# Performance work log

Hardware: AMD Instinct MI355X
Metric: run time of the kernel (lower is better)

Reference implementation:

```python
import jax, jax.numpy as jnp
import numpy as np

NPOINT = 2048
RADIUS = 0.2
NSAMPLE = 64
BN_EPS = 1e-5
MLP = [131, 128, 128, 256]  # 128 features + 3 xyz -> 128 -> 128 -> 256


def fps(xyz, npoint):
    """Furthest point sampling. xyz: (B,N,3) -> inds (B,npoint) int32. First index is 0 (CUDA convention)."""
    B, N, _ = xyz.shape
    dist0 = jnp.full((B, N), 1e10, dtype=xyz.dtype)
    idx0 = jnp.zeros((B,), dtype=jnp.int32)

    def step(carry, _):
        dist, last = carry
        last_pt = jnp.take_along_axis(xyz, last[:, None, None].astype(jnp.int32), axis=1)  # (B,1,3)
        d = jnp.sum((xyz - last_pt) ** 2, axis=-1)  # (B,N)
        dist = jnp.minimum(dist, d)
        nxt = jnp.argmax(dist, axis=1).astype(jnp.int32)
        return (dist, nxt), nxt

    (_, _), rest = jax.lax.scan(step, (dist0, idx0), None, length=npoint - 1)
    return jnp.concatenate([idx0[None, :], rest], axis=0).T  # (B,npoint)


def ball_query(all_xyz, new_xyz, radius, nsample):
    """For each query pick the first (lowest-index) nsample points within radius; pad with first hit.
    all_xyz: (B,Np,3), new_xyz: (B,S,3) -> idx (B,S,nsample) int32."""
    Np = all_xyz.shape[1]
    d2 = jnp.sum((new_xyz[:, :, None, :] - all_xyz[:, None, :, :]) ** 2, axis=-1)  # (B,S,Np)
    key = jnp.where(d2 < radius * radius, jnp.arange(Np, dtype=jnp.int32)[None, None, :], Np)
    topk = -jax.lax.top_k(-key, nsample)[0]  # nsample smallest indices, ascending
    valid = topk < Np
    first = topk[..., :1]
    idx = jnp.where(valid, topk, first)
    return jnp.where(idx >= Np, 0, idx).astype(jnp.int32)


def bn_relu(x, gamma, beta):
    # training-mode BatchNorm over (B,S,K) per channel (last axis), biased variance
    mean = jnp.mean(x, axis=(0, 1, 2), keepdims=True)
    var = jnp.mean((x - mean) ** 2, axis=(0, 1, 2), keepdims=True)
    return jax.nn.relu((x - mean) * jax.lax.rsqrt(var + BN_EPS) * gamma + beta)


def setup_inputs() -> dict:
    key = jax.random.key(0)
    ks = jax.random.split(key, 10)
    B, N, M, C = 4, 16384, 256, 128
    fixed_xyz = jax.random.uniform(ks[0], (B, M, 3), dtype=jnp.float32)
    xyz = jax.random.uniform(ks[1], (B, N, 3), dtype=jnp.float32)
    features = jax.random.normal(ks[2], (B, C, M + N), dtype=jnp.float32)
    W1 = jax.random.normal(ks[3], (MLP[1], MLP[0]), dtype=jnp.float32) * 0.05
    W2 = jax.random.normal(ks[4], (MLP[2], MLP[1]), dtype=jnp.float32) * 0.05
    W3 = jax.random.normal(ks[5], (MLP[3], MLP[2]), dtype=jnp.float32) * 0.05
    g1 = jnp.ones((MLP[1],), jnp.float32); b1 = jnp.zeros((MLP[1],), jnp.float32)
    g2 = jnp.ones((MLP[2],), jnp.float32); b2 = jnp.zeros((MLP[2],), jnp.float32)
    g3 = jnp.ones((MLP[3],), jnp.float32); b3 = jnp.zeros((MLP[3],), jnp.float32)
    return {"fixed_xyz": fixed_xyz, "xyz": xyz, "features": features,
            "W1": W1, "g1": g1, "b1": b1, "W2": W2, "g2": g2, "b2": b2,
            "W3": W3, "g3": g3, "b3": b3}


def reference(fixed_xyz, xyz, features, W1, g1, b1, W2, g2, b2, W3, g3, b3):
    B = xyz.shape[0]
    # FPS on the raw cloud, gather sampled centers, prepend fixed seeds
    inds = fps(xyz, NPOINT)  # (B,npoint)
    sampled = jnp.take_along_axis(xyz, inds[:, :, None], axis=1)  # (B,npoint,3)
    new_xyz = jnp.concatenate([fixed_xyz, sampled], axis=1)       # (B,S,3)
    all_xyz = jnp.concatenate([fixed_xyz, xyz], axis=1)           # (B,Np,3)

    idx = ball_query(all_xyz, new_xyz, RADIUS, NSAMPLE)           # (B,S,K)
    b = jnp.arange(B)[:, None, None]
    grouped_xyz = all_xyz[b, idx] - new_xyz[:, :, None, :]        # (B,S,K,3)
    grouped_xyz = grouped_xyz / RADIUS                            # normalize_xyz=True
    feats_t = jnp.transpose(features, (0, 2, 1))                  # (B,Np,C)
    grouped_feats = feats_t[b, idx]                               # (B,S,K,C)
    h = jnp.concatenate([grouped_xyz, grouped_feats], axis=-1)    # (B,S,K,3+C)

    # Shared MLP: 1x1 conv (no bias) + BN + ReLU per layer
    h = bn_relu(jnp.einsum('bskc,oc->bsko', h, W1), g1, b1)
    h = bn_relu(jnp.einsum('bskc,oc->bsko', h, W2), g2, b2)
    h = bn_relu(jnp.einsum('bskc,oc->bsko', h, W3), g3, b3)

    # max pool over the K (nsample) axis -> (B,Cout,S)
    new_features = jnp.transpose(jnp.max(h, axis=2), (0, 2, 1))
    return new_xyz, new_features, inds
```

## Files before the change

kernel.cpp:

```cpp
#include <hip/hip_runtime.h>
#include <hip/hip_bf16.h>
#include <cstdint>
#include <cstddef>

#define NB 4
#define N_PTS 16384
#define M_FIX 256
#define P_ALL 16640
#define S_TOT 2304
#define NPT 2048
#define KNB 64
#define CH1 128
#define CH3 256
#define NRED 589824.0f
#define ZPB (P_ALL / 64)

typedef float v2f __attribute__((ext_vector_type(2)));

#define OUT_XYZ 0
#define OUT_FEAT 27648
#define OUT_INDS 2386944

#define OFF_ALLX   0ull
#define OFF_STATS  798720ull
#define OFF_BN     1060864ull
#define OFF_MAXZ   1064960ull
#define OFF_MINZ   10502144ull
#define OFF_IDX    19939328ull
#define OFF_ZP     22298624ull
#define OFF_NEWX   39337984ull
#define OFF_INDSI  39448576ull
#define OFF_HIST   1064960ull
#define OFF_OFFS   1073152ull
#define OFF_SX     1081344ull
#define OFF_SY     1343488ull
#define OFF_SZ     1605632ull
#define OFF_SIDX   1867776ull
#define OFF_XYZ4   2129920ull

__device__ __forceinline__ float red16s(float v) {
  v += __shfl_xor(v, 1); v += __shfl_xor(v, 2);
  v += __shfl_xor(v, 4); v += __shfl_xor(v, 8);
  return v;
}
__device__ __forceinline__ float red16mx(float v) {
  v = fmaxf(v, __shfl_xor(v, 1)); v = fmaxf(v, __shfl_xor(v, 2));
  v = fmaxf(v, __shfl_xor(v, 4)); v = fmaxf(v, __shfl_xor(v, 8));
  return v;
}
__device__ __forceinline__ float red16mn(float v) {
  v = fminf(v, __shfl_xor(v, 1)); v = fminf(v, __shfl_xor(v, 2));
  v = fminf(v, __shfl_xor(v, 4)); v = fminf(v, __shfl_xor(v, 8));
  return v;
}
__device__ __forceinline__ float xyzp(float dx, float dy, float dz,
                                      float wx, float wy, float wz) {
  return fmaf(dx, wx, fmaf(dy, wy, __fmul_rn(dz, wz)));
}
__device__ __forceinline__ int mort3(int v) {
  return (v & 1) | ((v & 2) << 1) | ((v & 4) << 2);
}
__device__ __forceinline__ int cell_code(float x, float y, float z) {
  int cx = min(7, max(0, (int)(x * 8.0f)));
  int cy = min(7, max(0, (int)(y * 8.0f)));
  int cz = min(7, max(0, (int)(z * 8.0f)));
  return mort3(cx) | (mort3(cy) << 1) | (mort3(cz) << 2);
}

template <int CTRL, int RM>
__device__ __forceinline__ unsigned long long dppmax(unsigned long long k) {
  int lo = (int)(unsigned)(k & 0xFFFFFFFFull);
  int hi = (int)(unsigned)(k >> 32);
  int sl = __builtin_amdgcn_update_dpp(lo, lo, CTRL, RM, 0xF, false);
  int sh = __builtin_amdgcn_update_dpp(hi, hi, CTRL, RM, 0xF, false);
  unsigned long long s = ((unsigned long long)(unsigned)sh << 32) | (unsigned)sl;
  return (s > k) ? s : k;
}
__device__ __forceinline__ unsigned long long wave_max64(unsigned long long k) {
  k = dppmax<0x111, 0xF>(k);
  k = dppmax<0x112, 0xF>(k);
  k = dppmax<0x114, 0xF>(k);
  k = dppmax<0x118, 0xF>(k);
  k = dppmax<0x142, 0xa>(k);
  k = dppmax<0x143, 0xc>(k);
  return k;
}
__device__ __forceinline__ unsigned long long row_max64(unsigned long long k) {
  k = dppmax<0x111, 0xF>(k);
  k = dppmax<0x112, 0xF>(k);
  k = dppmax<0x114, 0xF>(k);
  k = dppmax<0x118, 0xF>(k);
  return k;
}

__global__ void k_build(const float* __restrict__ fixed, const float* __restrict__ xyz,
                        float* __restrict__ allx, float* __restrict__ newx,
                        float* __restrict__ stats, int* __restrict__ inds_i,
                        int* __restrict__ hist, float4* __restrict__ xyz4) {
  int i = blockIdx.x * 256 + threadIdx.x;
  if (i < NB * P_ALL * 3) {
    int b = i / (P_ALL * 3);
    int r = i % (P_ALL * 3);
    int p = r / 3, c = r % 3;
    float v = (p < M_FIX) ? fixed[((size_t)b * M_FIX + p) * 3 + c]
                          : xyz[((size_t)b * N_PTS + (p - M_FIX)) * 3 + c];
    allx[i] = v;
  }
  if (i < NB * N_PTS) {
    const float* pt = xyz + (size_t)i * 3;
    xyz4[i] = make_float4(pt[0], pt[1], pt[2], 0.f);
  }
  if (i < NB * M_FIX * 3) {
    int b = i / (M_FIX * 3);
    int r = i % (M_FIX * 3);
    newx[(size_t)b * S_TOT * 3 + r] = fixed[(size_t)b * M_FIX * 3 + r];
  }
  if (i < 65536) stats[i] = 0.0f;
  if (i < NB * 512) hist[i] = 0;
  if (i < NB) inds_i[(size_t)i * NPT] = 0;
}

__global__ void k_cell(const float* __restrict__ xyz, int* __restrict__ hist) {
  int i = blockIdx.x * 256 + threadIdx.x;
  int b = i >> 14;
  const float* pt = xyz + (size_t)i * 3;
  int code = cell_code(pt[0], pt[1], pt[2]);
  atomicAdd(&hist[(b << 9) + code], 1);
}

__global__ __launch_bounds__(512) void k_scan(const int* __restrict__ hist,
                                              int* __restrict__ offs) {
  __shared__ int tmp[512];
  int b = blockIdx.x, t = threadIdx.x;
  int h = hist[(b << 9) + t];
  tmp[t] = h;
  __syncthreads();
  for (int o = 1; o < 512; o <<= 1) {
    int v = (t >= o) ? tmp[t - o] : 0;
    __syncthreads();
    tmp[t] += v;
    __syncthreads();
  }
  offs[(b << 9) + t] = tmp[t] - h;
}

__global__ void k_scatter(const float* __restrict__ xyz, int* __restrict__ offs,
                          float* __restrict__ sx, float* __restrict__ sy,
                          float* __restrict__ sz, int* __restrict__ sidx) {
  int i = blockIdx.x * 256 + threadIdx.x;
  int b = i >> 14, p = i & 16383;
  const float* pt = xyz + (size_t)i * 3;
  float x = pt[0], y = pt[1], z = pt[2];
  int code = cell_code(x, y, z);
  int pos = atomicAdd(&offs[(b << 9) + code], 1);
  int o = (b << 14) + pos;
  sx[o] = x; sy[o] = y; sz[o] = z; sidx[o] = p;
}

__global__ __launch_bounds__(1024, 4) void k_fps(const float4* __restrict__ xyz4,
                                                 const float* __restrict__ sx,
                                                 const float* __restrict__ sy,
                                                 const float* __restrict__ sz,
                                                 const int* __restrict__ sidx,
                                                 float* __restrict__ newx,
                                                 int* __restrict__ inds_i,
                                                 const float* __restrict__ feats,
                                                 const float* __restrict__ W1,
                                                 __hip_bfloat16* __restrict__ zp) {
  __shared__ __align__(16) float smem[CH1 * 68 + 32 * 132];
  int t = threadIdx.x;

  if (blockIdx.x >= NB) {
    int bz = blockIdx.x - NB;
    int b = bz / ZPB;
    int p0 = (bz % ZPB) * 64;
    float* a_t = smem;
    float* w_t = smem + CH1 * 68;
    for (int r = t; r < CH1 * 64; r += 1024) {
      int c = r >> 6, p = r & 63;
      a_t[c * 68 + p] = feats[((size_t)b * CH1 + c) * P_ALL + p0 + p];
    }
    int tk = t & 63, to = t >> 6;
    v2f acc[4];
#pragma unroll
    for (int p = 0; p < 4; ++p) acc[p] = (v2f){0.f, 0.f};
    const float* Wg = W1 + 3;
    for (int c0 = 0; c0 < CH1; c0 += 32) {
      __syncthreads();
      for (int r = t; r < 32 * 128; r += 1024) {
        int o = r & 127, c = r >> 7;
        w_t[c * 132 + o] = Wg[(size_t)o * 131 + (c0 + c)];
      }
      __syncthreads();
#pragma unroll 4
      for (int c = 0; c < 32; ++c) {
        float a = a_t[(c0 + c) * 68 + tk];
        v2f w2[4];
        *(float4*)&w2[0] = *(const float4*)&w_t[c * 132 + to * 8];
        *(float4*)&w2[2] = *(const float4*)&w_t[c * 132 + to * 8 + 4];
        v2f a2 = {a, a};
#pragma unroll
        for (int p = 0; p < 4; ++p)
          acc[p] = __builtin_elementwise_fma(a2, w2[p], acc[p]);
      }
    }
    union { __hip_bfloat16 h[8]; uint4 u; } tmp;
#pragma unroll
    for (int j = 0; j < 8; ++j)
      tmp.h[j] = __float2bfloat16((j & 1) ? acc[j >> 1].y : acc[j >> 1].x);
    *(uint4*)&zp[((size_t)b * P_ALL + p0 + tk) * CH1 + to * 8] = tmp.u;
    return;
  }

  unsigned long long* red = (unsigned long long*)smem;
  float4* wcoord = (float4*)(smem + 32);
  float4* s_win = (float4*)(smem + 96);
  int* idxbuf = (int*)(smem + 100);

  int b = blockIdx.x;
  const float4* bx4 = xyz4 + (size_t)b * N_PTS;
  int off0 = (b << 14) + (t << 4);
  v2f px2[8], py2[8], pz2[8];
  float dist[16];
  unsigned npidp[8];
#pragma unroll
  for (int u = 0; u < 8; ++u) {
    px2[u] = *(const v2f*)&sx[off0 + 2 * u];
    py2[u] = *(const v2f*)&sy[off0 + 2 * u];
    pz2[u] = *(const v2f*)&sz[off0 + 2 * u];
    dist[2 * u] = 1e10f; dist[2 * u + 1] = 1e10f;
  }
#pragma unroll
  for (int u = 0; u < 8; ++u) {
    unsigned a = 16383u - (unsigned)sidx[off0 + 2 * u];
    unsigned c = 16383u - (unsigned)sidx[off0 + 2 * u + 1];
    npidp[u] = a | (c << 16);
  }
  float xmn = px2[0].x, xmx = px2[0].x, ymn = py2[0].x, ymx = py2[0].x;
  float zmn = pz2[0].x, zmx = pz2[0].x;
#pragma unroll
  for (int u = 0; u < 8; ++u) {
    xmn = fminf(xmn, fminf(px2[u].x, px2[u].y));
    xmx = fmaxf(xmx, fmaxf(px2[u].x, px2[u].y));
    ymn = fminf(ymn, fminf(py2[u].x, py2[u].y));
    ymx = fmaxf(ymx, fmaxf(py2[u].x, py2[u].y));
    zmn = fminf(zmn, fminf(pz2[u].x, pz2[u].y));
    zmx = fmaxf(zmx, fmaxf(pz2[u].x, pz2[u].y));
  }
  float cx = (xmn + xmx) * 0.5f, cy = (ymn + ymx) * 0.5f, cz = (zmn + zmx) * 0.5f;
  float r2m = 0.f;
#pragma unroll
  for (int u = 0; u < 8; ++u) {
#pragma unroll
    for (int h = 0; h < 2; ++h) {
      float ax = (h ? px2[u].y : px2[u].x) - cx;
      float ay = (h ? py2[u].y : py2[u].x) - cy;
      float az = (h ? pz2[u].y : pz2[u].x) - cz;
      r2m = fmaxf(r2m, ax * ax + ay * ay + az * az);
    }
  }
  float rad = sqrtf(r2m) + 2e-3f;
  float4 p0 = bx4[0];
  float lx = p0.x, ly = p0.y, lz = p0.z;
  if (t == 0) {
    size_t nb0 = ((size_t)b * S_TOT + M_FIX) * 3;
    newx[nb0] = lx; newx[nb0 + 1] = ly; newx[nb0 + 2] = lz;
  }
  unsigned long long bestkey = 0ull;
  unsigned long long kprev = ~0ull;
  float thr = 3.4e38f;
  int lane = t & 63, wid = t >> 6;
  for (int iter = 1; iter < NPT; ++iter) {
    float ex = lx - cx, ey = ly - cy, ez = lz - cz;
    bool active = (ex * ex + ey * ey + ez * ez) < thr;
    if (__ballot(active) != 0ull) {
      bool ch = false;
      if (active) {
#pragma clang fp contract(off)
        v2f l2x = {lx, lx}, l2y = {ly, ly}, l2z = {lz, lz};
#pragma unroll
        for (int u = 0; u < 8; ++u) {
          v2f dx = px2[u] - l2x;
          v2f dy = py2[u] - l2y;
          v2f dz = pz2[u] - l2z;
          v2f xx = dx * dx;
          v2f yy = dy * dy;
          v2f zz = dz * dz;
          v2f d2 = (xx + yy) + zz;
          if (d2.x < dist[2 * u])     { dist[2 * u] = d2.x;     ch = true; }
          if (d2.y < dist[2 * u + 1]) { dist[2 * u + 1] = d2.y; ch = true; }
        }
      }
      if (__ballot(ch) != 0ull) {
        if (ch) {
          unsigned long long c0 = 0ull, c1 = 0ull, c2 = 0ull, c3 = 0ull;
#pragma unroll
          for (int j = 0; j < 16; ++j) {
            unsigned lo16 = (j & 1) ? (npidp[j >> 1] >> 16) : (npidp[j >> 1] & 0xFFFFu);
            unsigned long long kj =
                ((unsigned long long)__float_as_uint(dist[j]) << 32) | lo16;
            if ((j & 3) == 0) c0 = (kj > c0) ? kj : c0;
            else if ((j & 3) == 1) c1 = (kj > c1) ? kj : c1;
            else if ((j & 3) == 2) c2 = (kj > c2) ? kj : c2;
            else c3 = (kj > c3) ? kj : c3;
          }
          c0 = (c1 > c0) ? c1 : c0;
          c2 = (c3 > c2) ? c3 : c2;
          bestkey = (c2 > c0) ? c2 : c0;
          float ub = __uint_as_float((unsigned)(bestkey >> 32));
          float tq = sqrtf(ub) + rad;
          thr = tq * tq;
        }
        unsigned long long k = wave_max64(bestkey);
        unsigned long long kall = __shfl(k, 63);
        if (kall != kprev) {
          if (bestkey == kall) {
            unsigned lo = (unsigned)(kall & 0xFFFFull);
            float wx = 0.f, wy = 0.f, wz = 0.f;
#pragma unroll
            for (int u = 0; u < 8; ++u) {
              unsigned pk = npidp[u];
              if ((pk & 0xFFFFu) == lo) { wx = px2[u].x; wy = py2[u].x; wz = pz2[u].x; }
              if ((pk >> 16) == lo)     { wx = px2[u].y; wy = py2[u].y; wz = pz2[u].y; }
            }
            wcoord[wid] = make_float4(wx, wy, wz, 0.f);
          }
          kprev = kall;
        }
        if (lane == 63) red[wid] = k;
      }
    }
    __syncthreads();
    if (wid == 0) {
      unsigned long long wk = red[lane & 15];
      unsigned long long wr = row_max64(wk);
      unsigned long long wmax = __shfl(wr, 15);
      unsigned long long mb = __ballot(wk == wmax) & 0xFFFFull;
      int src = __ffsll(mb) - 1;
      if (lane == 15) {
        *s_win = wcoord[src];
        idxbuf[iter] = 16383 - (int)(wmax & 0xFFFFull);
      }
    }
    __syncthreads();
    float4 wv = *s_win;
    lx = wv.x; ly = wv.y; lz = wv.z;
  }
  __syncthreads();
  for (int s = t; s < NPT; s += 1024) {
    if (s == 0) continue;
    int wi = idxbuf[s];
    float4 wp = bx4[wi];
    inds_i[(size_t)b * NPT + s] = wi;
    size_t nb2 = ((size_t)b * S_TOT + M_FIX + s) * 3;
    newx[nb2] = wp.x; newx[nb2 + 1] = wp.y; newx[nb2 + 2] = wp.z;
  }
}

__global__ __launch_bounds__(256) void k_ball(const float* __restrict__ allx,
                                              const float* __restrict__ newx,
                                              int* __restrict__ idx) {
  int wid = threadIdx.x >> 6, lane = threadIdx.x & 63;
  int q = blockIdx.x * 4 + wid;
  int b = q / S_TOT;
  const float* qp = newx + (size_t)q * 3;
  float qx = qp[0], qy = qp[1], qz = qp[2];
  const float* pts = allx + (size_t)b * P_ALL * 3;
  int* outp = idx + (size_t)q * KNB;
  const float R2 = 0.04f;
  int collected = 0;
  int first_hit = 0;
  for (int ch = 0; ch < P_ALL / 64; ++ch) {
    int p = ch * 64 + lane;
    float x = pts[p * 3 + 0], y = pts[p * 3 + 1], z = pts[p * 3 + 2];
    float dx = __fsub_rn(qx, x), dy = __fsub_rn(qy, y), dz = __fsub_rn(qz, z);
    float d2 = __fadd_rn(__fadd_rn(__fmul_rn(dx, dx), __fmul_rn(dy, dy)), __fmul_rn(dz, dz));
    bool hit = d2 < R2;
    unsigned long long m = __ballot(hit);
    if (m) {
      if (collected == 0) first_hit = ch * 64 + (__ffsll((unsigned long long)m) - 1);
      if (hit) {
        int slot = collected + __popcll(m & ((1ull << lane) - 1ull));
        if (slot < KNB) outp[slot] = p;
      }
      collected += __popcll(m);
      if (collected >= KNB) break;
    }
  }
  int sl = collected + lane;
  if (sl < KNB) outp[sl] = first_hit;
}

__device__ __forceinline__ void gemm_chunks(const float* a_t, float* w_t,
                                            const float* __restrict__ Wg, int K,
                                            int obase, int ldw, int tid,
                                            v2f acc[4][4]) {
  int tk = tid & 15, to = tid >> 4;
  for (int c0 = 0; c0 < K; c0 += 32) {
    __syncthreads();
    for (int r = tid; r < 32 * 128; r += 256) {
      int o = r & 127, c = r >> 7;
      w_t[c * 132 + o] = Wg[(size_t)(obase + o) * ldw + (c0 + c)];
    }
    __syncthreads();
#pragma unroll 4
    for (int c = 0; c < 32; ++c) {
      float a4[4];
      v2f w2[4];
      *(float4*)a4 = *(const float4*)&a_t[(c0 + c) * 68 + tk * 4];
      *(float4*)&w2[0] = *(const float4*)&w_t[c * 132 + to * 8];
      *(float4*)&w2[2] = *(const float4*)&w_t[c * 132 + to * 8 + 4];
#pragma unroll
      for (int i = 0; i < 4; ++i) {
        v2f a2 = {a4[i], a4[i]};
#pragma unroll
        for (int p = 0; p < 4; ++p)
          acc[i][p] = __builtin_elementwise_fma(a2, w2[p], acc[i][p]);
      }
    }
  }
}
#define ACC_J(acc, i, j) (((j) & 1) ? acc[i][(j) >> 1].y : acc[i][(j) >> 1].x)

__device__ __forceinline__ void stage_geom(int bs, int b, const int* __restrict__ idxg,
                                           const float* __restrict__ allx,
                                           const float* __restrict__ newx,
                                           const float* __restrict__ W1,
                                           int* s_pid, float* s_d, float* s_w1, int tid) {
  if (tid < 64) {
    int p = idxg[(size_t)bs * KNB + tid];
    s_pid[tid] = p;
    const float* pp = allx + ((size_t)b * P_ALL + p) * 3;
    const float* qq = newx + (size_t)bs * 3;
    s_d[tid]       = __fmul_rn(__fsub_rn(pp[0], qq[0]), 5.0f);
    s_d[64 + tid]  = __fmul_rn(__fsub_rn(pp[1], qq[1]), 5.0f);
    s_d[128 + tid] = __fmul_rn(__fsub_rn(pp[2], qq[2]), 5.0f);
  } else if (tid < 192) {
    int c = tid - 64;
    s_w1[c]       = W1[(size_t)c * 131 + 0];
    s_w1[128 + c] = W1[(size_t)c * 131 + 1];
    s_w1[256 + c] = W1[(size_t)c * 131 + 2];
  }
  __syncthreads();
}

__global__ __launch_bounds__(256) void k_stats1(const int* __restrict__ idxg,
                                                const float* __restrict__ allx,
                                                const float* __restrict__ newx,
                                                const float* __restrict__ W1,
                                                const __hip_bfloat16* __restrict__ zp,
                                                float* __restrict__ sSum,
                                                float* __restrict__ sSq) {
  __shared__ float smem[640 + 512];
  int* s_pid = (int*)smem;
  float* s_d = smem + 64;
  float* s_w1 = smem + 256;
  float* red = smem + 640;
  int bs = blockIdx.x;
  int b = bs / S_TOT;
  int tid = threadIdx.x;
  stage_geom(bs, b, idxg, allx, newx, W1, s_pid, s_d, s_w1, tid);
  int g = tid >> 7, c = tid & 127;
  float wx = s_w1[c], wy = s_w1[128 + c], wz = s_w1[256 + c];
  const uint16_t* zpb = (const uint16_t*)zp + (size_t)b * P_ALL * CH1;
  float s1 = 0.f, s2 = 0.f;
  for (int k = g; k < KNB; k += 2) {
    int pid = s_pid[k];
    float v = __uint_as_float(((unsigned)zpb[(size_t)pid * CH1 + c]) << 16);
    v += xyzp(s_d[k], s_d[64 + k], s_d[128 + k], wx, wy, wz);
    s1 += v; s2 = fmaf(v, v, s2);
  }
  red[tid] = s1;
  __syncthreads();
  float t1 = (tid < 128) ? red[tid] + red[tid + 128] : 0.f;
  __syncthreads();
  red[tid] = s2;
  __syncthreads();
  if (tid < 128) {
    float t2 = red[tid] + red[tid + 128];
    int slot = bs & 63;
    atomicAdd(&sSum[slot * CH1 + tid], t1);
    atomicAdd(&sSq[slot * CH1 + tid], t2);
  }
}

__device__ __forceinline__ void build_a1(float* a_t, const int* s_pid, const float* s_d,
                                         const float* s_w1,
                                         const __hip_bfloat16* __restrict__ zp_b,
                                         const float* __restrict__ bnS,
                                         const float* __restrict__ bnH, int tid) {
  int k = tid & 63, q = tid >> 6;
  int pid = s_pid[k];
  float dx = s_d[k], dy = s_d[64 + k], dz = s_d[128 + k];
  const uint32_t* zr = (const uint32_t*)((const uint16_t*)zp_b + (size_t)pid * CH1 + q * 32);
#pragma unroll
  for (int u = 0; u < 16; ++u) {
    uint32_t w = zr[u];
    int c = q * 32 + u * 2;
    float v0 = __uint_as_float(w << 16);
    float v1 = __uint_as_float(w & 0xFFFF0000u);
    v0 += xyzp(dx, dy, dz, s_w1[c], s_w1[128 + c], s_w1[256 + c]);
    v1 += xyzp(dx, dy, dz, s_w1[c + 1], s_w1[128 + c + 1], s_w1[256 + c + 1]);
    a_t[c * 68 + k]       = fmaxf(fmaf(v0, bnS[c], bnH[c]), 0.0f);
    a_t[(c + 1) * 68 + k] = fmaxf(fmaf(v1, bnS[c + 1], bnH[c + 1]), 0.0f);
  }
}

__global__ __launch_bounds__(256) void k_layer2s(const int* __restrict__ idxg,
                                                 const float* __restrict__ allx,
                                                 const float* __restrict__ newx,
                                                 const float* __restrict__ W1,
                                                 const __hip_bfloat16* __restrict__ zp,
                                                 const float* __restrict__ bn1S,
                                                 const float* __restrict__ bn1H,
                                                 const float* __restrict__ W2,
                                                 float* __restrict__ sSum,
                                                 float* __restrict__ sSq) {
  __shared__ __align__(16) float smem[CH1 * 68 + 32 * 132];
  float* a_t = smem;
  float* w_t = smem + CH1 * 68;
  int* s_pid = (int*)w_t;
  float* s_d = w_t + 64;
  float* s_w1 = w_t + 256;
  int bs = blockIdx.x;
  int b = bs / S_TOT;
  int tid = threadIdx.x;
  stage_geom(bs, b, idxg, allx, newx, W1, s_pid, s_d, s_w1, tid);
  build_a1(a_t, s_pid, s_d, s_w1, zp + (size_t)b * P_ALL * CH1, bn1S, bn1H, tid);
  v2f acc[4][4];
#pragma unroll
  for (int i = 0; i < 4; ++i)
#pragma unroll
    for (int p = 0; p < 4; ++p) acc[i][p] = (v2f){0.f, 0.f};
  gemm_chunks(a_t, w_t, W2, CH1, 0, CH1, tid, acc);
  int tk = tid & 15, to = tid >> 4;
  int slot = bs & 63;
#pragma unroll
  for (int j = 0; j < 8; ++j) {
    float s1 = 0.f, s2 = 0.f;
#pragma unroll
    for (int i = 0; i < 4; ++i) { float v = ACC_J(acc, i, j); s1 += v; s2 = fmaf(v, v, s2); }
    s1 = red16s(s1);
    s2 = red16s(s2);
    if (tk == 0) {
      int o = to * 8 + j;
      atomicAdd(&sSum[slot * CH1 + o], s1);
      atomicAdd(&sSq[slot * CH1 + o], s2);
    }
  }
}

__global__ __launch_bounds__(256) void k_layer3(const int* __restrict__ idxg,
                                                const float* __restrict__ allx,
                                                const float* __restrict__ newx,
                                                const float* __restrict__ W1,
                                                const __hip_bfloat16* __restrict__ zp,
                                                const float* __restrict__ bn1S,
                                                const float* __restrict__ bn1H,
                                                const float* __restrict__ W2,
                                                const float* __restrict__ bn2S,
                                                const float* __restrict__ bn2H,
                                                const float* __restrict__ W3,
                                                float* __restrict__ maxz,
                                                float* __restrict__ minz,
                                                float* __restrict__ sSum,
                                                float* __restrict__ sSq) {
  __shared__ __align__(16) float smem[CH1 * 68 + 32 * 132];
  float* a_t = smem;
  float* w_t = smem + CH1 * 68;
  int* s_pid = (int*)w_t;
  float* s_d = w_t + 64;
  float* s_w1 = w_t + 256;
  int bs = blockIdx.x;
  int b = bs / S_TOT;
  int tid = threadIdx.x;
  stage_geom(bs, b, idxg, allx, newx, W1, s_pid, s_d, s_w1, tid);
  build_a1(a_t, s_pid, s_d, s_w1, zp + (size_t)b * P_ALL * CH1, bn1S, bn1H, tid);
  v2f acc[4][4];
#pragma unroll
  for (int i = 0; i < 4; ++i)
#pragma unroll
    for (int p = 0; p < 4; ++p) acc[i][p] = (v2f){0.f, 0.f};
  gemm_chunks(a_t, w_t, W2, CH1, 0, CH1, tid, acc);
  int tk = tid & 15, to = tid >> 4;
  __syncthreads();
#pragma unroll
  for (int j = 0; j < 8; ++j) {
    int o = to * 8 + j;
    float sc = bn2S[o], sh = bn2H[o];
#pragma unroll
    for (int i = 0; i < 4; ++i)
      a_t[o * 68 + tk * 4 + i] = fmaxf(fmaf(ACC_J(acc, i, j), sc, sh), 0.0f);
  }
  int slot = bs & 63;
#pragma unroll 1
  for (int half = 0; half < 2; ++half) {
    v2f acc3[4][4];
#pragma unroll
    for (int i = 0; i < 4; ++i)
#pragma unroll
      for (int p = 0; p < 4; ++p) acc3[i][p] = (v2f){0.f, 0.f};
    gemm_chunks(a_t, w_t, W3, CH1, half * 128, CH1, tid, acc3);
#pragma unroll
    for (int j = 0; j < 8; ++j) {
      float s1 = 0.f, s2 = 0.f, mx = -3.4e38f, mn = 3.4e38f;
#pragma unroll
      for (int i = 0; i < 4; ++i) {
        float v = ACC_J(acc3, i, j);
        s1 += v; s2 = fmaf(v, v, s2);
        mx = fmaxf(mx, v); mn = fminf(mn, v);
      }
      s1 = red16s(s1);
      s2 = red16s(s2);
      mx = red16mx(mx);
      mn = red16mn(mn);
      if (tk == 0) {
        int o = half * 128 + to * 8 + j;
        atomicAdd(&sSum[slot * CH3 + o], s1);
        atomicAdd(&sSq[slot * CH3 + o], s2);
        size_t base = (size_t)bs * CH3 + o;
        maxz[base] = mx;
        minz[base] = mn;
      }
    }
  }
}

__global__ void k_fin(const float* __restrict__ sSum, const float* __restrict__ sSq,
                      const float* __restrict__ gamma, const float* __restrict__ beta,
                      float* __restrict__ bnS, float* __restrict__ bnH, int C) {
  int o = threadIdx.x;
  if (o >= C) return;
  float s1 = 0.f, s2 = 0.f;
  for (int t = 0; t < 64; ++t) { s1 += sSum[t * C + o]; s2 += sSq[t * C + o]; }
  float mean = s1 / NRED;
  float var = fmaxf(s2 / NRED - mean * mean, 0.f);
  float inv = 1.0f / sqrtf(var + 1e-5f);
  float sc = gamma[o] * inv;
  bnS[o] = sc;
  bnH[o] = beta[o] - mean * sc;
}

__global__ __launch_bounds__(256) void k_final(const float* __restrict__ maxz,
                                               const float* __restrict__ minz,
                                               const float* __restrict__ bnS,
                                               const float* __restrict__ bnH,
                                               float* __restrict__ out) {
  int bs = blockIdx.x;
  int o = threadIdx.x;
  float sc = bnS[o], sh = bnH[o];
  size_t base = (size_t)bs * CH3 + o;
  float v = (sc >= 0.f) ? maxz[base] : minz[base];
  float r = fmaxf(fmaf(v, sc, sh), 0.f);
  int b = bs / S_TOT, s = bs % S_TOT;
  out[OUT_FEAT + ((size_t)b * CH3 + o) * S_TOT + s] = r;
}

__global__ void k_copy(const float* __restrict__ newx, const int* __restrict__ inds_i,
                       float* __restrict__ out) {
  int i = blockIdx.x * 256 + threadIdx.x;
  if (i < NB * S_TOT * 3) out[OUT_XYZ + i] = newx[i];
  else {
    int r = i - NB * S_TOT * 3;
    if (r < NB * NPT) out[OUT_INDS + r] = (float)inds_i[r];
  }
}

extern "C" void kernel_launch(void* const* d_in, const int* in_sizes, int n_in,
                              void* d_out, int out_size, void* d_ws, size_t ws_size,
                              hipStream_t stream) {
  const float* fixed = (const float*)d_in[0];
  const float* xyz = (const float*)d_in[1];
  const float* feats = (const float*)d_in[2];
  const float* W1 = (const float*)d_in[3];
  const float* g1 = (const float*)d_in[4];
  const float* b1 = (const float*)d_in[5];
  const float* W2 = (const float*)d_in[6];
  const float* g2 = (const float*)d_in[7];
  const float* b2 = (const float*)d_in[8];
  const float* W3 = (const float*)d_in[9];
  const float* g3 = (const float*)d_in[10];
  const float* b3 = (const float*)d_in[11];
  float* out = (float*)d_out;

  char* w = (char*)d_ws;
  float* allx = (float*)(w + OFF_ALLX);
  float* newx = (float*)(w + OFF_NEWX);
  int* inds_i = (int*)(w + OFF_INDSI);
  int* idx = (int*)(w + OFF_IDX);
  float* stats = (float*)(w + OFF_STATS);
  float* s1sum = stats, *s1sq = stats + 8192;
  float* s2sum = stats + 16384, *s2sq = stats + 24576;
  float* s3sum = stats + 32768, *s3sq = stats + 49152;
  float* bn = (float*)(w + OFF_BN);
  float* bn1s = bn, *bn1h = bn + 128;
  float* bn2s = bn + 256, *bn2h = bn + 384;
  float* bn3s = bn + 512, *bn3h = bn + 768;
  float* maxz = (float*)(w + OFF_MAXZ);
  float* minz = (float*)(w + OFF_MINZ);
  __hip_bfloat16* zp = (__hip_bfloat16*)(w + OFF_ZP);
  int* hist = (int*)(w + OFF_HIST);
  int* offs = (int*)(w + OFF_OFFS);
  float* sxp = (float*)(w + OFF_SX);
  float* syp = (float*)(w + OFF_SY);
  float* szp = (float*)(w + OFF_SZ);
  int* sidx = (int*)(w + OFF_SIDX);
  float4* xyz4 = (float4*)(w + OFF_XYZ4);

  k_build<<<(NB * P_ALL * 3 + 255) / 256, 256, 0, stream>>>(fixed, xyz, allx, newx, stats, inds_i, hist, xyz4);
  k_cell<<<NB * N_PTS / 256, 256, 0, stream>>>(xyz, hist);
  k_scan<<<NB, 512, 0, stream>>>(hist, offs);
  k_scatter<<<NB * N_PTS / 256, 256, 0, stream>>>(xyz, offs, sxp, syp, szp, sidx);
  k_fps<<<NB + NB * ZPB, 1024, 0, stream>>>(xyz4, sxp, syp, szp, sidx, newx, inds_i,
                                            feats, W1, zp);
  k_ball<<<(NB * S_TOT) / 4, 256, 0, stream>>>(allx, newx, idx);
  k_stats1<<<NB * S_TOT, 256, 0, stream>>>(idx, allx, newx, W1, zp, s1sum, s1sq);
  k_fin<<<1, 256, 0, stream>>>(s1sum, s1sq, g1, b1, bn1s, bn1h, 128);
  k_layer2s<<<NB * S_TOT, 256, 0, stream>>>(idx, allx, newx, W1, zp, bn1s, bn1h, W2, s2sum, s2sq);
  k_fin<<<1, 256, 0, stream>>>(s2sum, s2sq, g2, b2, bn2s, bn2h, 128);
  k_layer3<<<NB * S_TOT, 256, 0, stream>>>(idx, allx, newx, W1, zp, bn1s, bn1h, W2,
                                           bn2s, bn2h, W3, maxz, minz, s3sum, s3sq);
  k_fin<<<1, 256, 0, stream>>>(s3sum, s3sq, g3, b3, bn3s, bn3h, 256);
  k_final<<<NB * S_TOT, 256, 0, stream>>>(maxz, minz, bn3s, bn3h, out);
  k_copy<<<(NB * S_TOT * 3 + NB * NPT + 255) / 256, 256, 0, stream>>>(newx, inds_i, out);
}
```

Baseline: 4.587 ms.

## Double-buffer FPS cross-wave reduction to drop a barrier; fuse copy into final kernel

The FPS loop now has every wave redundantly reduce the 16 per-wave maxima from a double-buffered shared array, which removes the second __syncthreads and the wave-0 broadcast step in each of the 2047 iterations. Owner waves keep their winning coordinate in registers and write it after the branch. Separately, the k_copy kernel is folded into k_final as extra blocks, saving one launch. The trade-off is that every wave now does the redundant LDS reads and DPP reduction. Inactive waves also republish stale keys, which relies on kw and is_owner persisting correctly across iterations.

```diff
diff --git a/kernel.cpp b/kernel.cpp
--- a/kernel.cpp
+++ b/kernel.cpp
@@ -212,10 +212,9 @@
     return;
   }
 
-  unsigned long long* red = (unsigned long long*)smem;
-  float4* wcoord = (float4*)(smem + 32);
-  float4* s_win = (float4*)(smem + 96);
-  int* idxbuf = (int*)(smem + 100);
+  unsigned long long* red2 = (unsigned long long*)smem;
+  float4* wcoord2 = (float4*)(smem + 64);
+  int* idxbuf = (int*)(smem + 192);
 
   int b = blockIdx.x;
   const float4* bx4 = xyz4 + (size_t)b * N_PTS;
@@ -267,9 +266,13 @@
     newx[nb0] = lx; newx[nb0 + 1] = ly; newx[nb0 + 2] = lz;
   }
   unsigned long long bestkey = 0ull;
+  unsigned long long kw = 0ull;
   unsigned long long kprev = ~0ull;
+  bool is_owner = false;
+  float4 mywin = make_float4(0.f, 0.f, 0.f, 0.f);
   float thr = 3.4e38f;
   int lane = t & 63, wid = t >> 6;
+  int cur = 0;
   for (int iter = 1; iter < NPT; ++iter) {
     float ex = lx - cx, ey = ly - cy, ez = lz - cz;
     bool active = (ex * ex + ey * ey + ez * ez) < thr;
@@ -311,10 +314,11 @@
           float tq = sqrtf(ub) + rad;
           thr = tq * tq;
         }
-        unsigned long long k = wave_max64(bestkey);
-        unsigned long long kall = __shfl(k, 63);
+        kw = wave_max64(bestkey);
+        unsigned long long kall = __shfl(kw, 63);
         if (kall != kprev) {
-          if (bestkey == kall) {
+          is_owner = (bestkey == kall);
+          if (is_owner) {
             unsigned lo = (unsigned)(kall & 0xFFFFull);
             float wx = 0.f, wy = 0.f, wz = 0.f;
 #pragma unroll
@@ -323,28 +327,24 @@
               if ((pk & 0xFFFFu) == lo) { wx = px2[u].x; wy = py2[u].x; wz = pz2[u].x; }
               if ((pk >> 16) == lo)     { wx = px2[u].y; wy = py2[u].y; wz = pz2[u].y; }
             }
-            wcoord[wid] = make_float4(wx, wy, wz, 0.f);
+            mywin = make_float4(wx, wy, wz, 0.f);
           }
           kprev = kall;
         }
-        if (lane == 63) red[wid] = k;
       }
     }
+    if (lane == 63) red2[cur * 16 + wid] = kw;
+    if (is_owner) wcoord2[cur * 16 + wid] = mywin;
     __syncthreads();
-    if (wid == 0) {
-      unsigned long long wk = red[lane & 15];
-      unsigned long long wr = row_max64(wk);
-      unsigned long long wmax = __shfl(wr, 15);
-      unsigned long long mb = __ballot(wk == wmax) & 0xFFFFull;
-      int src = __ffsll(mb) - 1;
-      if (lane == 15) {
-        *s_win = wcoord[src];
-        idxbuf[iter] = 16383 - (int)(wmax & 0xFFFFull);
-      }
-    }
-    __syncthreads();
-    float4 wv = *s_win;
+    unsigned long long wk = red2[cur * 16 + (lane & 15)];
+    unsigned long long wr = row_max64(wk);
+    unsigned long long wmax = __shfl(wr, 15);
+    unsigned long long mb = __ballot(wk == wmax) & 0xFFFFull;
+    int src = __ffsll(mb) - 1;
+    float4 wv = wcoord2[cur * 16 + src];
     lx = wv.x; ly = wv.y; lz = wv.z;
+    if (t == 0) idxbuf[iter] = 16383 - (int)(wmax & 0xFFFFull);
+    cur ^= 1;
   }
   __syncthreads();
   for (int s = t; s < NPT; s += 1024) {
@@ -645,7 +645,18 @@
                                                const float* __restrict__ minz,
                                                const float* __restrict__ bnS,
                                                const float* __restrict__ bnH,
+                                               const float* __restrict__ newx,
+                                               const int* __restrict__ inds_i,
                                                float* __restrict__ out) {
+  if (blockIdx.x >= NB * S_TOT) {
+    int i = (blockIdx.x - NB * S_TOT) * 256 + threadIdx.x;
+    if (i < NB * S_TOT * 3) out[OUT_XYZ + i] = newx[i];
+    else {
+      int r = i - NB * S_TOT * 3;
+      if (r < NB * NPT) out[OUT_INDS + r] = (float)inds_i[r];
+    }
+    return;
+  }
   int bs = blockIdx.x;
   int o = threadIdx.x;
   float sc = bnS[o], sh = bnH[o];
@@ -654,16 +665,6 @@
   float r = fmaxf(fmaf(v, sc, sh), 0.f);
   int b = bs / S_TOT, s = bs % S_TOT;
   out[OUT_FEAT + ((size_t)b * CH3 + o) * S_TOT + s] = r;
-}
-
-__global__ void k_copy(const float* __restrict__ newx, const int* __restrict__ inds_i,
-                       float* __restrict__ out) {
-  int i = blockIdx.x * 256 + threadIdx.x;
-  if (i < NB * S_TOT * 3) out[OUT_XYZ + i] = newx[i];
-  else {
-    int r = i - NB * S_TOT * 3;
-    if (r < NB * NPT) out[OUT_INDS + r] = (float)inds_i[r];
-  }
 }
 
 extern "C" void kernel_launch(void* const* d_in, const int* in_sizes, int n_in,
@@ -721,6 +722,5 @@
   k_layer3<<<NB * S_TOT, 256, 0, stream>>>(idx, allx, newx, W1, zp, bn1s, bn1h, W2,
                                            bn2s, bn2h, W3, maxz, minz, s3sum, s3sq);
   k_fin<<<1, 256, 0, stream>>>(s3sum, s3sq, g3, b3, bn3s, bn3h, 256);
-  k_final<<<NB * S_TOT, 256, 0, stream>>>(maxz, minz, bn3s, bn3h, out);
-  k_copy<<<(NB * S_TOT * 3 + NB * NPT + 255) / 256, 256, 0, stream>>>(newx, inds_i, out);
-}
+  k_final<<<NB * S_TOT + 140, 256, 0, stream>>>(maxz, minz, bn3s, bn3h, newx, inds_i, out);
+}
```

New measurement: 4.646 ms. No clear change (+1.3%).
